# Kernel tuning notes

Measured on AMD Instinct MI355X. Metric: run time of the kernel, lower is better.

Reference implementation:

```python
import jax, jax.numpy as jnp
import numpy as np

N_NODES = 100000
N_EDGES = 1600000
IN_DIM = 64
H0, H1, H2 = 128, 128, 256
OUT_DIM = 40


def setup_inputs() -> dict:
    key = jax.random.key(0)
    ks = jax.random.split(key, 10)
    features = jax.random.normal(ks[0], (N_NODES, IN_DIM), dtype=jnp.float32)
    edge_index = jax.random.randint(ks[1], (2, N_EDGES), 0, N_NODES, dtype=jnp.int64)
    def lin(k, fan_in, fan_out):
        s = 1.0 / np.sqrt(fan_in)
        return jax.random.uniform(k, (fan_in, fan_out), jnp.float32, -s, s)
    # GraphSAGE-mean layers: W acts on concat([self, mean_neigh]) -> 2*in_dim
    W1 = lin(ks[2], 2 * IN_DIM, H0)
    b1 = jnp.zeros((H0,), jnp.float32)
    W2 = lin(ks[3], 2 * H0, H1)
    b2 = jnp.zeros((H1,), jnp.float32)
    # MLP classifier
    Wm1 = lin(ks[4], H1, H2)
    bm1 = jnp.zeros((H2,), jnp.float32)
    Wm2 = lin(ks[5], H2, OUT_DIM)
    bm2 = jnp.zeros((OUT_DIM,), jnp.float32)
    return {"features": features, "edge_index": edge_index,
            "W1": W1, "b1": b1, "W2": W2, "b2": b2,
            "Wm1": Wm1, "bm1": bm1, "Wm2": Wm2, "bm2": bm2}


def _sage_layer(x, src, dst, W, b, n_nodes):
    # gather source-node features along edges, mean-aggregate at destinations
    msgs = x[src]                                             # [E, d]
    agg = jax.ops.segment_sum(msgs, dst, num_segments=n_nodes)  # [N, d]
    cnt = jax.ops.segment_sum(jnp.ones((src.shape[0], 1), x.dtype), dst,
                              num_segments=n_nodes)            # [N, 1]
    neigh = agg / jnp.maximum(cnt, 1.0)
    return jnp.concatenate([x, neigh], axis=-1) @ W + b


def reference(features, edge_index, W1, b1, W2, b2, Wm1, bm1, Wm2, bm2):
    src, dst = edge_index[0], edge_index[1]
    n = features.shape[0]
    h = jax.nn.sigmoid(_sage_layer(features, src, dst, W1, b1, n))
    h = jax.nn.sigmoid(_sage_layer(h, src, dst, W2, b2, n))
    # MLP (dropout is identity at inference, batch_norm=False)
    h = jax.nn.relu(h @ Wm1 + bm1)
    return h @ Wm2 + bm2
```

## Files before the change

kernel.cpp:

```cpp
#include <hip/hip_runtime.h>
#include <math.h>


typedef unsigned short u16;
typedef unsigned int u32;

#define CAP 64

using frag_ab = __attribute__((ext_vector_type(8))) short;
using frag_cd = __attribute__((ext_vector_type(4))) float;

__device__ __forceinline__ float b2f(u16 u) { return __uint_as_float(((u32)u) << 16); }
__device__ __forceinline__ u16 f2b(float f) {
    u32 u = __float_as_uint(f);
    u += 0x7fffu + ((u >> 16) & 1u);
    return (u16)(u >> 16);
}

__global__ __launch_bounds__(64) void k_detect(const void* edges, int* flag) {
    if (threadIdx.x == 0 && blockIdx.x == 0) {
        const int* w = (const int*)edges;
        int o = 0;
        for (int i = 1; i < 128; i += 2) o |= w[i];
        *flag = (o == 0) ? 1 : 0;
    }
}

__device__ __forceinline__ int edge_at(const void* p, int is64, size_t idx) {
    return is64 ? (int)((const long long*)p)[idx] : ((const int*)p)[idx];
}

__global__ __launch_bounds__(256) void k_fill_slots(const void* edges,
                                                    const int* flag, int E,
                                                    int* cnt, int* slots,
                                                    int* ovf, int* ovf_cnt) {
    int is64 = *flag;
    for (int e = blockIdx.x * blockDim.x + threadIdx.x; e < E;
         e += gridDim.x * blockDim.x) {
        int s = edge_at(edges, is64, (size_t)e);
        int d = edge_at(edges, is64, (size_t)E + e);
        int pos = atomicAdd(&cnt[d], 1);
        if (pos < CAP) {
            slots[(size_t)d * CAP + pos] = s;
        } else {
            int op = atomicAdd(ovf_cnt, 1);
            ovf[2 * op] = d;
            ovf[2 * op + 1] = s;
        }
    }
}

__global__ __launch_bounds__(256) void k_cvt(const float* __restrict__ in,
                                             u16* __restrict__ out, int cnt4) {
    int i = blockIdx.x * blockDim.x + threadIdx.x;
    if (i < cnt4) {
        float4 v = reinterpret_cast<const float4*>(in)[i];
        ushort4 o;
        o.x = f2b(v.x); o.y = f2b(v.y); o.z = f2b(v.z); o.w = f2b(v.w);
        reinterpret_cast<ushort4*>(out)[i] = o;
    }
}

template <int D>
__global__ __launch_bounds__(256) void k_agg16(const u16* __restrict__ x,
                                               const int* __restrict__ cnt,
                                               const int* __restrict__ slots,
                                               const int* __restrict__ ovf,
                                               const int* __restrict__ ovf_cnt,
                                               u16* __restrict__ outn, int n) {
    constexpr int V = D / 64;
    int node = blockIdx.x * 4 + (threadIdx.x >> 6);
    int lane = threadIdx.x & 63;
    if (node >= n) return;
    int c = cnt[node];
    int m = c < CAP ? c : CAP;
    const int* sl = slots + (size_t)node * CAP;
    float acc[V];
#pragma unroll
    for (int i = 0; i < V; ++i) acc[i] = 0.f;

    int e = 0;
    for (; e + 3 < m; e += 4) {
        int sA = sl[e], sB = sl[e + 1], sC = sl[e + 2], sD = sl[e + 3];
        if (V == 1) {
            float a0 = b2f(x[(size_t)sA * 64 + lane]);
            float a1 = b2f(x[(size_t)sB * 64 + lane]);
            float a2 = b2f(x[(size_t)sC * 64 + lane]);
            float a3 = b2f(x[(size_t)sD * 64 + lane]);
            acc[0] += (a0 + a1) + (a2 + a3);
        } else {
            u32 u0 = *reinterpret_cast<const u32*>(x + (size_t)sA * 128 + lane * 2);
            u32 u1 = *reinterpret_cast<const u32*>(x + (size_t)sB * 128 + lane * 2);
            u32 u2 = *reinterpret_cast<const u32*>(x + (size_t)sC * 128 + lane * 2);
            u32 u3 = *reinterpret_cast<const u32*>(x + (size_t)sD * 128 + lane * 2);
            acc[0] += (b2f((u16)u0) + b2f((u16)u1)) + (b2f((u16)u2) + b2f((u16)u3));
            acc[1] += (b2f((u16)(u0 >> 16)) + b2f((u16)(u1 >> 16))) +
                      (b2f((u16)(u2 >> 16)) + b2f((u16)(u3 >> 16)));
        }
    }
    for (; e < m; ++e) {
        int sA = sl[e];
        if (V == 1) {
            acc[0] += b2f(x[(size_t)sA * 64 + lane]);
        } else {
            u32 u0 = *reinterpret_cast<const u32*>(x + (size_t)sA * 128 + lane * 2);
            acc[0] += b2f((u16)u0);
            acc[1] += b2f((u16)(u0 >> 16));
        }
    }
    if (c > CAP) {
        int mo = *ovf_cnt;
        for (int i = 0; i < mo; ++i) {
            if (ovf[2 * i] == node) {
                int sA = ovf[2 * i + 1];
                if (V == 1) {
                    acc[0] += b2f(x[(size_t)sA * 64 + lane]);
                } else {
                    u32 u0 = *reinterpret_cast<const u32*>(x + (size_t)sA * 128 + lane * 2);
                    acc[0] += b2f((u16)u0);
                    acc[1] += b2f((u16)(u0 >> 16));
                }
            }
        }
    }
    float inv = 1.0f / (float)(c > 0 ? c : 1);
    if (V == 1) {
        outn[(size_t)node * 64 + lane] = f2b(acc[0] * inv);
    } else {
        u32 o = (u32)f2b(acc[0] * inv) | ((u32)f2b(acc[1] * inv) << 16);
        *reinterpret_cast<u32*>(outn + (size_t)node * 128 + lane * 2) = o;
    }
}

template <int K1, int K2, int NT, int ACT>
__global__ __launch_bounds__(256) void k_gemm16(const u16* __restrict__ A1,
                                                const u16* __restrict__ A2,
                                                const float* __restrict__ W,
                                                const float* __restrict__ bias,
                                                u16* __restrict__ C, int M) {
    constexpr int K = K1 + K2;
    __shared__ u16 Wt[128 * K];
    const int tid = threadIdx.x;
    const int m0 = blockIdx.x * 128;
    const int n0 = blockIdx.y * 128;

    for (int idx = tid; idx < K * 64; idx += 256) {
        int c = idx & 127;
        int kp = idx >> 7;
        float w0 = W[(size_t)(2 * kp) * NT + n0 + c];
        float w1 = W[(size_t)(2 * kp + 1) * NT + n0 + c];
        u32 pk = (u32)f2b(w0) | ((u32)f2b(w1) << 16);
        int byte = c * (K * 2) + kp * 4;
        byte ^= (c & 7) << 4;
        *reinterpret_cast<u32*>(reinterpret_cast<char*>(Wt) + byte) = pk;
    }
    __syncthreads();

    const int wid = tid >> 6, lane = tid & 63;
    const int wr = (wid >> 1) * 64;
    const int wc = (wid & 1) * 64;
    const int lr = lane & 15;
    const int lk = (lane >> 4) * 8;

    frag_cd acc[4][4];
#pragma unroll
    for (int mt = 0; mt < 4; ++mt)
#pragma unroll
        for (int nt = 0; nt < 4; ++nt)
            acc[mt][nt] = (frag_cd){0.f, 0.f, 0.f, 0.f};

#pragma unroll 4
    for (int k0 = 0; k0 < K; k0 += 32) {
        const int k = k0 + lk;
        frag_ab b[4];
#pragma unroll
        for (int nt = 0; nt < 4; ++nt) {
            int c = wc + nt * 16 + lr;
            int byte = c * (K * 2) + k * 2;
            byte ^= (c & 7) << 4;
            b[nt] = *reinterpret_cast<const frag_ab*>(
                reinterpret_cast<const char*>(Wt) + byte);
        }
        frag_ab a[4];
#pragma unroll
        for (int mt = 0; mt < 4; ++mt) {
            int r = m0 + wr + mt * 16 + lr;
            if (r >= M) r = M - 1;
            const u16* p = (K2 == 0 || k < K1)
                               ? (A1 + (size_t)r * K1 + k)
                               : (A2 + (size_t)r * K2 + (k - K1));
            a[mt] = *reinterpret_cast<const frag_ab*>(p);
        }
#pragma unroll
        for (int mt = 0; mt < 4; ++mt)
#pragma unroll
            for (int nt = 0; nt < 4; ++nt)
                acc[mt][nt] = __builtin_amdgcn_mfma_f32_16x16x32_bf16(
                    a[mt], b[nt], acc[mt][nt], 0, 0, 0);
    }

    const int orow = (lane >> 4) * 4;
#pragma unroll
    for (int mt = 0; mt < 4; ++mt) {
#pragma unroll
        for (int nt = 0; nt < 4; ++nt) {
            int col = n0 + wc + nt * 16 + lr;
            float bb = bias[col];
#pragma unroll
            for (int r = 0; r < 4; ++r) {
                int row = m0 + wr + mt * 16 + orow + r;
                if (row < M) {
                    float v = acc[mt][nt][r] + bb;
                    if (ACT == 1) v = 1.0f / (1.0f + __expf(-v));
                    else if (ACT == 2) v = v > 0.f ? v : 0.f;
                    C[(size_t)row * NT + col] = f2b(v);
                }
            }
        }
    }
}

__global__ __launch_bounds__(256) void k_out(const u16* __restrict__ h3,
                                             const float* __restrict__ Wm2,
                                             const float* __restrict__ bm2,
                                             float* __restrict__ out, int M) {
    constexpr int K = 256, NO = 40, BM = 32;
    __shared__ float As[BM][129];
    __shared__ float Ws[128 * NO];
    int tid = threadIdx.x;
    int m0 = blockIdx.x * BM;
    int r = tid >> 3;
    int cg = tid & 7;
    float acc[5] = {0.f, 0.f, 0.f, 0.f, 0.f};
    for (int kh = 0; kh < 2; ++kh) {
        for (int i = tid; i < BM * 64; i += 256) {
            int rr = i >> 6, j2 = i & 63;
            int row = m0 + rr;
            if (row >= M) row = M - 1;
            u32 u = *reinterpret_cast<const u32*>(h3 + (size_t)row * K + kh * 128 + j2 * 2);
            As[rr][j2 * 2] = b2f((u16)u);
            As[rr][j2 * 2 + 1] = b2f((u16)(u >> 16));
        }
        for (int i = tid; i < 128 * NO; i += 256) Ws[i] = Wm2[kh * 128 * NO + i];
        __syncthreads();
        for (int k = 0; k < 128; ++k) {
            float a = As[r][k];
#pragma unroll
            for (int j = 0; j < 5; ++j) acc[j] += a * Ws[k * NO + cg * 5 + j];
        }
        __syncthreads();
    }
    int row = m0 + r;
    if (row < M) {
#pragma unroll
        for (int j = 0; j < 5; ++j)
            out[(size_t)row * NO + cg * 5 + j] = acc[j] + bm2[cg * 5 + j];
    }
}

extern "C" void kernel_launch(void* const* d_in, const int* in_sizes, int n_in,
                              void* d_out, int out_size, void* d_ws, size_t ws_size,
                              hipStream_t stream) {
    const float* features = (const float*)d_in[0];
    const void* edges     = d_in[1];
    const float* W1  = (const float*)d_in[2];
    const float* b1  = (const float*)d_in[3];
    const float* W2  = (const float*)d_in[4];
    const float* b2  = (const float*)d_in[5];
    const float* Wm1 = (const float*)d_in[6];
    const float* bm1 = (const float*)d_in[7];
    const float* Wm2 = (const float*)d_in[8];
    const float* bm2 = (const float*)d_in[9];
    float* out = (float*)d_out;

    const int n = in_sizes[0] / 64;
    const int E = in_sizes[1] / 2;

    size_t off = 0;
    auto carve = [&](size_t bytes) {
        size_t cur = off;
        off += (bytes + 511) & ~(size_t)511;
        return cur;
    };
    char* ws = (char*)d_ws;
    int* cnt     = (int*)(ws + carve((size_t)n * 4));
    int* flag    = (int*)(ws + carve(64));
    int* ovf_cnt = (int*)(ws + carve(64));
    int* slots   = (int*)(ws + carve((size_t)n * CAP * 4));
    int* ovf     = (int*)(ws + carve((size_t)E * 2 * 4));
    u16* feat16    = (u16*)(ws + carve((size_t)n * 64 * 2));
    u16* neigh1_16 = (u16*)(ws + carve((size_t)n * 64 * 2));
    u16* h1_16     = (u16*)(ws + carve((size_t)n * 128 * 2));
    u16* neigh2_16 = (u16*)(ws + carve((size_t)n * 128 * 2));
    u16* h2_16     = (u16*)(ws + carve((size_t)n * 128 * 2));
    u16* h3_16     = feat16;

    hipMemsetAsync(cnt, 0, (size_t)n * 4, stream);
    hipMemsetAsync(ovf_cnt, 0, 4, stream);
    k_detect<<<1, 64, 0, stream>>>(edges, flag);
    k_fill_slots<<<4096, 256, 0, stream>>>(edges, flag, E, cnt, slots, ovf, ovf_cnt);

    const int cnt4 = n * 64 / 4;
    k_cvt<<<(cnt4 + 255) / 256, 256, 0, stream>>>(features, feat16, cnt4);

    const int aggGrid = (n + 3) / 4;
    const int gm = (n + 127) / 128;

    k_agg16<64><<<aggGrid, 256, 0, stream>>>(feat16, cnt, slots, ovf, ovf_cnt,
                                             neigh1_16, n);
    k_gemm16<64, 64, 128, 1><<<dim3(gm, 1), 256, 0, stream>>>(
        feat16, neigh1_16, W1, b1, h1_16, n);
    k_agg16<128><<<aggGrid, 256, 0, stream>>>(h1_16, cnt, slots, ovf, ovf_cnt,
                                              neigh2_16, n);
    k_gemm16<128, 128, 128, 1><<<dim3(gm, 1), 256, 0, stream>>>(
        h1_16, neigh2_16, W2, b2, h2_16, n);
    k_gemm16<128, 0, 256, 2><<<dim3(gm, 2), 256, 0, stream>>>(
        h2_16, nullptr, Wm1, bm1, h3_16, n);
    k_out<<<(n + 31) / 32, 256, 0, stream>>>(h3_16, Wm2, bm2, out, n);
}
```

Baseline: 570.0 us.

## Bin slot filling by destination range and unroll neighbor gather by eight

Slot filling now runs as eight passes, each keeping only edges whose destination falls in one node range. Atomics and slot writes then hit a smaller, cache-resident region. In exchange the edge list is re-read eight times and seven more kernels are launched. Slot capacity drops from 64 to 32, so more edges go to the overflow list, which every aggregation thread with an overflowing node scans linearly. The aggregation loop is unrolled by eight to keep more gathers in flight.

```diff
diff --git a/kernel.cpp b/kernel.cpp
--- a/kernel.cpp
+++ b/kernel.cpp
@@ -5,7 +5,8 @@
 typedef unsigned short u16;
 typedef unsigned int u32;
 
-#define CAP 64
+#define CAP 32
+#define NBINS 8
 
 using frag_ab = __attribute__((ext_vector_type(8))) short;
 using frag_cd = __attribute__((ext_vector_type(4))) float;
@@ -30,22 +31,25 @@
     return is64 ? (int)((const long long*)p)[idx] : ((const int*)p)[idx];
 }
 
-__global__ __launch_bounds__(256) void k_fill_slots(const void* edges,
-                                                    const int* flag, int E,
-                                                    int* cnt, int* slots,
-                                                    int* ovf, int* ovf_cnt) {
+__global__ __launch_bounds__(256) void k_fill_bin(const void* edges,
+                                                  const int* flag, int E,
+                                                  int lo, int hi,
+                                                  int* cnt, int* slots,
+                                                  int* ovf, int* ovf_cnt) {
     int is64 = *flag;
     for (int e = blockIdx.x * blockDim.x + threadIdx.x; e < E;
          e += gridDim.x * blockDim.x) {
-        int s = edge_at(edges, is64, (size_t)e);
         int d = edge_at(edges, is64, (size_t)E + e);
-        int pos = atomicAdd(&cnt[d], 1);
-        if (pos < CAP) {
-            slots[(size_t)d * CAP + pos] = s;
-        } else {
-            int op = atomicAdd(ovf_cnt, 1);
-            ovf[2 * op] = d;
-            ovf[2 * op + 1] = s;
+        if (d >= lo && d < hi) {
+            int s = edge_at(edges, is64, (size_t)e);
+            int pos = atomicAdd(&cnt[d], 1);
+            if (pos < CAP) {
+                slots[(size_t)d * CAP + pos] = s;
+            } else {
+                int op = atomicAdd(ovf_cnt, 1);
+                ovf[2 * op] = d;
+                ovf[2 * op + 1] = s;
+            }
         }
     }
 }
@@ -80,22 +84,43 @@
     for (int i = 0; i < V; ++i) acc[i] = 0.f;
 
     int e = 0;
+    for (; e + 7 < m; e += 8) {
+        int si[8];
+#pragma unroll
+        for (int j = 0; j < 8; ++j) si[j] = sl[e + j];
+        if (V == 1) {
+            float a[8];
+#pragma unroll
+            for (int j = 0; j < 8; ++j) a[j] = b2f(x[(size_t)si[j] * 64 + lane]);
+            acc[0] += ((a[0] + a[1]) + (a[2] + a[3])) + ((a[4] + a[5]) + (a[6] + a[7]));
+        } else {
+            u32 u[8];
+#pragma unroll
+            for (int j = 0; j < 8; ++j)
+                u[j] = *reinterpret_cast<const u32*>(x + (size_t)si[j] * 128 + lane * 2);
+            float lo = 0.f, hi = 0.f;
+#pragma unroll
+            for (int j = 0; j < 8; ++j) {
+                lo += b2f((u16)u[j]);
+                hi += b2f((u16)(u[j] >> 16));
+            }
+            acc[0] += lo; acc[1] += hi;
+        }
+    }
     for (; e + 3 < m; e += 4) {
-        int sA = sl[e], sB = sl[e + 1], sC = sl[e + 2], sD = sl[e + 3];
+        int si[4];
+#pragma unroll
+        for (int j = 0; j < 4; ++j) si[j] = sl[e + j];
         if (V == 1) {
-            float a0 = b2f(x[(size_t)sA * 64 + lane]);
-            float a1 = b2f(x[(size_t)sB * 64 + lane]);
-            float a2 = b2f(x[(size_t)sC * 64 + lane]);
-            float a3 = b2f(x[(size_t)sD * 64 + lane]);
-            acc[0] += (a0 + a1) + (a2 + a3);
+#pragma unroll
+            for (int j = 0; j < 4; ++j) acc[0] += b2f(x[(size_t)si[j] * 64 + lane]);
         } else {
-            u32 u0 = *reinterpret_cast<const u32*>(x + (size_t)sA * 128 + lane * 2);
-            u32 u1 = *reinterpret_cast<const u32*>(x + (size_t)sB * 128 + lane * 2);
-            u32 u2 = *reinterpret_cast<const u32*>(x + (size_t)sC * 128 + lane * 2);
-            u32 u3 = *reinterpret_cast<const u32*>(x + (size_t)sD * 128 + lane * 2);
-            acc[0] += (b2f((u16)u0) + b2f((u16)u1)) + (b2f((u16)u2) + b2f((u16)u3));
-            acc[1] += (b2f((u16)(u0 >> 16)) + b2f((u16)(u1 >> 16))) +
-                      (b2f((u16)(u2 >> 16)) + b2f((u16)(u3 >> 16)));
+#pragma unroll
+            for (int j = 0; j < 4; ++j) {
+                u32 u0 = *reinterpret_cast<const u32*>(x + (size_t)si[j] * 128 + lane * 2);
+                acc[0] += b2f((u16)u0);
+                acc[1] += b2f((u16)(u0 >> 16));
+            }
         }
     }
     for (; e < m; ++e) {
@@ -298,7 +323,14 @@
     hipMemsetAsync(cnt, 0, (size_t)n * 4, stream);
     hipMemsetAsync(ovf_cnt, 0, 4, stream);
     k_detect<<<1, 64, 0, stream>>>(edges, flag);
-    k_fill_slots<<<4096, 256, 0, stream>>>(edges, flag, E, cnt, slots, ovf, ovf_cnt);
+
+    const int binsz = (n + NBINS - 1) / NBINS;
+    for (int b = 0; b < NBINS; ++b) {
+        int lo = b * binsz;
+        int hi = lo + binsz < n ? lo + binsz : n;
+        k_fill_bin<<<2048, 256, 0, stream>>>(edges, flag, E, lo, hi,
+                                             cnt, slots, ovf, ovf_cnt);
+    }
 
     const int cnt4 = n * 64 / 4;
     k_cvt<<<(cnt4 + 255) / 256, 256, 0, stream>>>(features, feat16, cnt4);
```

New measurement: 522.3 us. 8.4% less time.
